# Kernel optimization log

Measured on AMD Instinct MI355X. Metric: run time of the kernel, lower is better.

## Reference

```python
import jax, jax.numpy as jnp
import numpy as np

L, B, D, N = 2048, 8, 1024, 64

def setup_inputs() -> dict:
    key = jax.random.key(0)
    ks = jax.random.split(key, 6)
    return {
        "x": jax.random.normal(ks[0], (L, B, D), dtype=jnp.float32),
        "damping_factor": jax.random.normal(ks[1], (D, N, 1), dtype=jnp.float32),
        "decay_factor": jax.random.normal(ks[2], (D, N, 1), dtype=jnp.float32),
        "ema_expansion_matrix": jax.random.normal(ks[3], (D, N, 1), dtype=jnp.float32),
        "kernel_projection_matrix": jax.random.normal(ks[4], (D, N), dtype=jnp.float32),
        "residual_weight": jax.random.normal(ks[5], (D,), dtype=jnp.float32),
    }

def reference(x, damping_factor, decay_factor, ema_expansion_matrix,
              kernel_projection_matrix, residual_weight):
    seq_len, bsz, dim = x.shape
    ndim = damping_factor.shape[1]
    # --- kernel synthesis (training path, unidirectional) ---
    damping = jax.nn.sigmoid(damping_factor)           # (D, N, 1)
    decay = jax.nn.sigmoid(decay_factor)               # (D, N, 1)
    prev_w = 1.0 - damping * decay                     # (D, N, 1), in (0,1)
    t = jnp.arange(seq_len, dtype=jnp.float32)[None, None, :]  # (1,1,L)
    vander = t * jnp.log(prev_w)                       # (D, N, L)
    kernel_vals = damping * ema_expansion_matrix * jnp.exp(vander)  # (D,N,L)
    kernel = jnp.einsum('dnl,dn->dl', kernel_vals, kernel_projection_matrix)
    kernel = kernel * np.float32(1.0 / np.sqrt(ndim))  # (D, L)
    # --- residual + FFT long convolution ---
    residual = x * residual_weight                     # (L, B, D)
    x_conv = jnp.transpose(x, (1, 2, 0))               # (B, D, L)
    n_fft = 2 * seq_len
    x_fft = jnp.fft.rfft(x_conv, n=n_fft)              # (B, D, n/2+1)
    k_fft = jnp.fft.rfft(kernel, n=n_fft)              # (D, n/2+1)
    conv = jnp.fft.irfft(x_fft * k_fft, n=n_fft)[..., :seq_len]  # (B, D, L)
    ema_out = jnp.transpose(conv, (2, 0, 1))           # (L, B, D)
    return jax.nn.silu(ema_out + residual)
```

## Files before the change

### kernel.cpp

```cpp
#include <hip/hip_runtime.h>
#include <hip/hip_bf16.h>


#define BSZ 8
#define DIM 1024
#define ND 64
#define BD 8192
#define SEGS 4
#define SEGLEN 512
#define CH1 64
#define CPS1 8
#define TD 16
#define XP1 68
#define NCH2 16
#define YP2 17

typedef short bf16x8 __attribute__((ext_vector_type(8)));
typedef float f32x4 __attribute__((ext_vector_type(4)));
union BF8 { uint32_t u[4]; bf16x8 v; };
#define MFMA __builtin_amdgcn_mfma_f32_16x16x32_bf16

__device__ __forceinline__ uint32_t pk_bf16(float a, float b) {
    __hip_bfloat162 h2 = __float22bfloat162_rn(make_float2(a, b));
    uint32_t u; __builtin_memcpy(&u, &h2, 4);
    return u;
}

__device__ __forceinline__ void block_sync_lds() {
    asm volatile("s_waitcnt lgkmcnt(0)" ::: "memory");
    __builtin_amdgcn_s_barrier();
    asm volatile("" ::: "memory");
}

__global__ __launch_bounds__(128, 8) void mega_pass1(
    const float* __restrict__ x,
    const float* __restrict__ dfp,
    const float* __restrict__ cfp,
    ushort* __restrict__ S)
{
    __shared__ float xb[2][TD * XP1];

    const int tid = threadIdx.x;
    const int lane = tid & 63;
    const int wv = tid >> 6;
    const int q   = (lane & 3) | (((lane >> 3) & 1) << 2);
    const int col = wv * 8 + ((lane >> 2) & 1) + ((lane >> 4) & 3) * 2;
    const int blk = blockIdx.x;
    const int dt  = blk & 63;
    const int b   = (blk >> 6) & 7;
    const int seg = blk >> 9;
    const int d   = dt * TD + col;

    float w[8];
    {
        const int pb = d * ND + q * 8;
        const float4 df0 = *(const float4*)(dfp + pb);
        const float4 df1 = *(const float4*)(dfp + pb + 4);
        const float4 cf0 = *(const float4*)(cfp + pb);
        const float4 cf1 = *(const float4*)(cfp + pb + 4);
        const float dfv[8] = {df0.x, df0.y, df0.z, df0.w, df1.x, df1.y, df1.z, df1.w};
        const float cfv[8] = {cf0.x, cf0.y, cf0.z, cf0.w, cf1.x, cf1.y, cf1.z, cf1.w};
        #pragma unroll
        for (int i = 0; i < 8; ++i) {
            const float sd = 1.0f / (1.0f + __expf(-dfv[i]));
            const float sc = 1.0f / (1.0f + __expf(-cfv[i]));
            w[i] = 1.0f - sd * sc;
        }
    }

    const int r0 = tid >> 2;
    const int c4 = (tid & 3) * 4;
    const float* xg = x + (size_t)(seg * SEGLEN) * BD + b * DIM + dt * TD;

    float4 nx0 = *(const float4*)(xg + (size_t)r0 * BD + c4);
    float4 nx1 = *(const float4*)(xg + (size_t)(r0 + 32) * BD + c4);

    float h[8];
    #pragma unroll
    for (int i = 0; i < 8; ++i) h[i] = 0.0f;

    for (int g = 0; g < CPS1; ++g) {
        float* xbuf = xb[g & 1];
        const float nv0[4] = {nx0.x, nx0.y, nx0.z, nx0.w};
        const float nv1[4] = {nx1.x, nx1.y, nx1.z, nx1.w};
        #pragma unroll
        for (int e = 0; e < 4; ++e) {
            xbuf[(c4 + e) * XP1 + r0]      = nv0[e];
            xbuf[(c4 + e) * XP1 + r0 + 32] = nv1[e];
        }
        if (g + 1 < CPS1) {
            nx0 = *(const float4*)(xg + (size_t)((g + 1) * CH1 + r0) * BD + c4);
            nx1 = *(const float4*)(xg + (size_t)((g + 1) * CH1 + r0 + 32) * BD + c4);
        }
        block_sync_lds();

        const float* xcol = xbuf + col * XP1;
        #pragma unroll 2
        for (int t8 = 0; t8 < 8; ++t8) {
            const float4 tva = *(const float4*)(xcol + t8 * 8);
            const float4 tvb = *(const float4*)(xcol + t8 * 8 + 4);
            const float tvs[8] = {tva.x, tva.y, tva.z, tva.w,
                                  tvb.x, tvb.y, tvb.z, tvb.w};
            #pragma unroll
            for (int k = 0; k < 8; ++k) {
                const float xv = tvs[k];
                #pragma unroll
                for (int i = 0; i < 8; ++i) h[i] = fmaf(w[i], h[i], xv);
            }
        }
    }

    const size_t sb = ((size_t)(seg * BSZ + b) * 64 + dt) * 1024 + col * 64 + q * 8;
    uint32_t pk[4] = {pk_bf16(h[0], h[1]), pk_bf16(h[2], h[3]),
                      pk_bf16(h[4], h[5]), pk_bf16(h[6], h[7])};
    *(uint4*)(S + sb) = make_uint4(pk[0], pk[1], pk[2], pk[3]);
}

__global__ __launch_bounds__(1024, 4) void mega_pass2(
    const float* __restrict__ x,
    const float* __restrict__ dfp,
    const float* __restrict__ cfp,
    const float* __restrict__ emp,
    const float* __restrict__ pjp,
    const float* __restrict__ rwp,
    const ushort* __restrict__ S,
    float* __restrict__ out)
{
    __shared__ __align__(16) float   xb[2][TD * 8 * 36];
    __shared__ __align__(16) float   yt[2][256 * YP2];
    __shared__ __align__(16) uint32_t hbq[16 * 256];
    __shared__ __align__(8)  float2  pclw[16 * 64];
    __shared__ float kap[16 * 32];

    const int tid = threadIdx.x;
    const int tl  = tid & 63;
    const int wv  = tid >> 6;
    const int c   = tl & 15;
    const int g   = tl >> 4;
    const int blk = blockIdx.x;
    const int seg = blk >> 6;
    const int dt  = blk & 63;
    const int d0  = dt * TD;
    const int d   = d0 + wv;

    {
        const int pidx = d * ND + tl;
        const float sd = 1.0f / (1.0f + __expf(-dfp[pidx]));
        const float sc = 1.0f / (1.0f + __expf(-cfp[pidx]));
        const float wn = 1.0f - sd * sc;
        const float cn = sd * emp[pidx] * pjp[pidx] * 0.125f;
        pclw[wv * 64 + tl] = make_float2(cn, log2f(wn));
    }
    const float rwd = rwp[d];

    const int rid = tid >> 2;
    const int l_s = rid >> 3;
    const int b_s = rid & 7;
    const int dq  = tid & 3;
    const float* xg_st = x + (size_t)(seg * SEGLEN + l_s) * BD + b_s * DIM + d0 + 4 * dq;
    float4 nx = *(const float4*)(xg_st);

    float lw16[16];
    #pragma unroll
    for (int T = 0; T < 4; ++T)
        #pragma unroll
        for (int r = 0; r < 4; ++r)
            lw16[T * 4 + r] = pclw[wv * 64 + 16 * T + 4 * g + r].y;

    float h[16];
    #pragma unroll
    for (int i = 0; i < 16; ++i) h[i] = 0.0f;
    if (seg > 0) {
        float w512[16];
        #pragma unroll
        for (int i = 0; i < 16; ++i) w512[i] = exp2f(512.0f * lw16[i]);
        for (int sp = 0; sp < seg; ++sp) {
            const size_t sbase = ((size_t)(sp * BSZ + (c & 7)) * 64 + dt) * 1024 + wv * 64;
            #pragma unroll
            for (int T = 0; T < 4; ++T) {
                const uint2 u = *(const uint2*)(S + sbase + 16 * T + 4 * g);
                const float s0 = __uint_as_float(u.x << 16);
                const float s1 = __uint_as_float(u.x & 0xFFFF0000u);
                const float s2 = __uint_as_float(u.y << 16);
                const float s3 = __uint_as_float(u.y & 0xFFFF0000u);
                h[T*4+0] = fmaf(w512[T*4+0], h[T*4+0], s0);
                h[T*4+1] = fmaf(w512[T*4+1], h[T*4+1], s1);
                h[T*4+2] = fmaf(w512[T*4+2], h[T*4+2], s2);
                h[T*4+3] = fmaf(w512[T*4+3], h[T*4+3], s3);
            }
        }
    }
    float w32[16];
    #pragma unroll
    for (int i = 0; i < 16; ++i) w32[i] = exp2f(32.0f * lw16[i]);

    BF8 Vf[4], T2f[2][2], Kf[2];
    #pragma unroll
    for (int T = 0; T < 4; ++T) {
        const float2 pcl = pclw[wv * 64 + 16 * T + c];
        const float winv = exp2f(-pcl.y);
        float ve = exp2f((float)(31 - 8 * g) * pcl.y);
        float vv[8];
        #pragma unroll
        for (int e = 0; e < 8; ++e) { vv[e] = ve; ve *= winv; }
        #pragma unroll
        for (int j = 0; j < 4; ++j) Vf[T].u[j] = pk_bf16(vv[2*j], vv[2*j+1]);
    }
    #pragma unroll
    for (int Tk = 0; Tk < 2; ++Tk) {
        float2 m8[8];
        #pragma unroll
        for (int e = 0; e < 8; ++e) m8[e] = pclw[wv * 64 + 32 * Tk + 8 * g + e];
        #pragma unroll
        for (int Tj = 0; Tj < 2; ++Tj) {
            const float jf = (float)(16 * Tj + c + 1);
            float tv[8];
            #pragma unroll
            for (int e = 0; e < 8; ++e) tv[e] = m8[e].x * exp2f(jf * m8[e].y);
            #pragma unroll
            for (int j = 0; j < 4; ++j) T2f[Tj][Tk].u[j] = pk_bf16(tv[2*j], tv[2*j+1]);
        }
    }
    {
        const int p = tl >> 1, half = tl & 1;
        float acc = 0.0f;
        for (int i = 0; i < 32; ++i) {
            const float2 pc = pclw[wv * 64 + half * 32 + i];
            acc = fmaf(pc.x, exp2f((float)p * pc.y), acc);
        }
        const int prt = __builtin_amdgcn_update_dpp(0, __float_as_int(acc), 0xB1, 0xF, 0xF, true);
        acc += __int_as_float(prt);
        if (!half) kap[wv * 32 + p] = acc;
    }
    #pragma unroll
    for (int Tj = 0; Tj < 2; ++Tj) {
        float kv[8];
        #pragma unroll
        for (int e = 0; e < 8; ++e) {
            const int pp = 16 * Tj + c - 8 * g - e;
            const float kr = kap[wv * 32 + (pp > 0 ? pp : 0)];
            kv[e] = (pp >= 0) ? kr : 0.0f;
        }
        #pragma unroll
        for (int j = 0; j < 4; ++j) Kf[Tj].u[j] = pk_bf16(kv[2*j], kv[2*j+1]);
    }

    const int swl  = (wv >> 2) & 3;
    const int swzc = ((c & 3) << 3) | (((c >> 2) & 1) << 2);
    uint32_t* hbw = hbq + wv * 256 + (c & 7) * 32;
    float* ogbase = out + (size_t)(seg * SEGLEN) * BD + d0;
    const f32x4 zf = {0.0f, 0.0f, 0.0f, 0.0f};

    const int yrho = b_s + 8 * ((l_s >> 2) & 3) + 32 * (l_s & 3) + 128 * (l_s >> 4);

    if (c < 8) {
        #pragma unroll
        for (int T = 0; T < 4; ++T) {
            const uint32_t u0 = pk_bf16(h[4*T+0], h[4*T+1]);
            const uint32_t u1 = pk_bf16(h[4*T+2], h[4*T+3]);
            *(uint2*)(&hbw[(8 * T + 2 * g) ^ swzc]) = make_uint2(u0, u1);
        }
    }
    {
        const float nv[4] = {nx.x, nx.y, nx.z, nx.w};
        #pragma unroll
        for (int e = 0; e < 4; ++e)
            xb[0][((4 * dq + e) * 8 + b_s) * 36 + (l_s ^ (dq << 3))] = nv[e];
        nx = *(const float4*)(xg_st + (size_t)32 * BD);
    }
    block_sync_lds();

    for (int ch = 0; ch < NCH2; ++ch) {
        float* xbuf = xb[ch & 1];
        const float* xrow = xbuf + (wv * 8 + (c & 7)) * 36;

        BF8 hB0, hB1;
        {
            const uint4 a = *(const uint4*)(&hbw[(4 * g) ^ swzc]);
            const uint4 b2 = *(const uint4*)(&hbw[(16 + 4 * g) ^ swzc]);
            hB0.u[0]=a.x; hB0.u[1]=a.y; hB0.u[2]=a.z; hB0.u[3]=a.w;
            hB1.u[0]=b2.x; hB1.u[1]=b2.y; hB1.u[2]=b2.z; hB1.u[3]=b2.w;
        }
        BF8 xB;
        {
            const int kb = (8 * g) ^ (swl << 3);
            const float4 fa = *(const float4*)(xrow + kb);
            const float4 fb = *(const float4*)(xrow + kb + 4);
            xB.u[0] = pk_bf16(fa.x, fa.y); xB.u[1] = pk_bf16(fa.z, fa.w);
            xB.u[2] = pk_bf16(fb.x, fb.y); xB.u[3] = pk_bf16(fb.z, fb.w);
        }

        if (ch + 1 < NCH2) {
            const float nv[4] = {nx.x, nx.y, nx.z, nx.w};
            #pragma unroll
            for (int e = 0; e < 4; ++e)
                xb[(ch + 1) & 1][((4 * dq + e) * 8 + b_s) * 36 + (l_s ^ (dq << 3))] = nv[e];
            if (ch + 2 < NCH2)
                nx = *(const float4*)(xg_st + (size_t)(ch + 2) * 32 * BD);
        }
        if (ch > 0) {
            const float* yprev = yt[(ch - 1) & 1];
            float ov[4];
            #pragma unroll
            for (int e = 0; e < 4; ++e) ov[e] = yprev[yrho * YP2 + 4 * dq + e];
            *(float4*)(ogbase + (size_t)((ch - 1) * 32 + l_s) * BD + b_s * DIM + 4 * dq) =
                make_float4(ov[0], ov[1], ov[2], ov[3]);
        }

        f32x4 y0 = MFMA(Kf[0].v, xB.v, zf, 0, 0, 0);
        f32x4 y1 = MFMA(Kf[1].v, xB.v, zf, 0, 0, 0);
        y0 = MFMA(T2f[0][0].v, hB0.v, y0, 0, 0, 0);
        y1 = MFMA(T2f[1][0].v, hB0.v, y1, 0, 0, 0);
        y0 = MFMA(T2f[0][1].v, hB1.v, y0, 0, 0, 0);
        y1 = MFMA(T2f[1][1].v, hB1.v, y1, 0, 0, 0);
        #pragma unroll
        for (int T = 0; T < 4; ++T) {
            const f32x4 U = MFMA(Vf[T].v, xB.v, zf, 0, 0, 0);
            h[4*T+0] = fmaf(w32[4*T+0], h[4*T+0], U[0]);
            h[4*T+1] = fmaf(w32[4*T+1], h[4*T+1], U[1]);
            h[4*T+2] = fmaf(w32[4*T+2], h[4*T+2], U[2]);
            h[4*T+3] = fmaf(w32[4*T+3], h[4*T+3], U[3]);
        }
        if (c < 8) {
            #pragma unroll
            for (int T = 0; T < 4; ++T) {
                const uint32_t u0 = pk_bf16(h[4*T+0], h[4*T+1]);
                const uint32_t u1 = pk_bf16(h[4*T+2], h[4*T+3]);
                *(uint2*)(&hbw[(8 * T + 2 * g) ^ swzc]) = make_uint2(u0, u1);
            }
        }

        float* ycur = yt[ch & 1];
        #pragma unroll
        for (int Tj = 0; Tj < 2; ++Tj) {
            const int jb = (16 * Tj + 4 * g) ^ (swl << 3);
            const float4 xres = *(const float4*)(xrow + jb);
            const float xr[4] = {xres.x, xres.y, xres.z, xres.w};
            const f32x4 yy = Tj ? y1 : y0;
            #pragma unroll
            for (int r = 0; r < 4; ++r) {
                const float v = yy[r] + rwd * xr[r];
                const float sv = v / (1.0f + __expf(-v));
                if (c < 8)
                    ycur[(c + 8 * (g + 4 * r + 16 * Tj)) * YP2 + wv] = sv;
            }
        }
        block_sync_lds();
    }

    {
        const float* yprev = yt[(NCH2 - 1) & 1];
        float ov[4];
        #pragma unroll
        for (int e = 0; e < 4; ++e) ov[e] = yprev[yrho * YP2 + 4 * dq + e];
        *(float4*)(ogbase + (size_t)((NCH2 - 1) * 32 + l_s) * BD + b_s * DIM + 4 * dq) =
            make_float4(ov[0], ov[1], ov[2], ov[3]);
    }
}

extern "C" void kernel_launch(void* const* d_in, const int* in_sizes, int n_in,
                              void* d_out, int out_size, void* d_ws, size_t ws_size,
                              hipStream_t stream) {
    const float* x  = (const float*)d_in[0];
    const float* df = (const float*)d_in[1];
    const float* cf = (const float*)d_in[2];
    const float* em = (const float*)d_in[3];
    const float* pj = (const float*)d_in[4];
    const float* rw = (const float*)d_in[5];
    float* out = (float*)d_out;
    ushort* S  = (ushort*)d_ws;

    mega_pass1<<<dim3((SEGS - 1) * BSZ * 64), dim3(128), 0, stream>>>(x, df, cf, S);
    mega_pass2<<<dim3(SEGS * 64), dim3(1024), 0, stream>>>(x, df, cf, em, pj, rw, S, out);
}
```

Baseline: 79.04 us.

## Process two 32-step chunks per iteration using idle MFMA column halves

The pass-2 loop now handles 64 timesteps per iteration instead of 32, filling the previously unused upper 8 MFMA columns (c>=8) with a second chunk. The state carry between the two half-chunks is passed via DPP lane moves, and the hidden-state buffer layout and swizzles are reworked. The aim is to halve the loop trip count and barriers and to double useful MFMA work per instruction. In exchange it adds a serial dependency inside each iteration, more LDS usage and extra barrier placement that may lower occupancy.

```diff
diff --git a/kernel.cpp b/kernel.cpp
--- a/kernel.cpp
+++ b/kernel.cpp
@@ -12,8 +12,7 @@
 #define CPS1 8
 #define TD 16
 #define XP1 68
-#define NCH2 16
-#define YP2 17
+#define NIT 8
 
 typedef short bf16x8 __attribute__((ext_vector_type(8)));
 typedef float f32x4 __attribute__((ext_vector_type(4)));
@@ -26,11 +25,18 @@
     return u;
 }
 
+template <int CTRL>
+__device__ __forceinline__ float dpp_mov(float v) {
+    return __int_as_float(__builtin_amdgcn_update_dpp(0, __float_as_int(v), CTRL, 0xF, 0xF, true));
+}
+
 __device__ __forceinline__ void block_sync_lds() {
     asm volatile("s_waitcnt lgkmcnt(0)" ::: "memory");
     __builtin_amdgcn_s_barrier();
     asm volatile("" ::: "memory");
 }
+
+#define HB_ADDR(cc, p0) ((((p0) >> 4) * 256) + ((((p0) >> 2) & 3) * 64) + ((cc) * 4) + ((p0) & 3))
 
 __global__ __launch_bounds__(128, 8) void mega_pass1(
     const float* __restrict__ x,
@@ -126,10 +132,10 @@
     const ushort* __restrict__ S,
     float* __restrict__ out)
 {
-    __shared__ __align__(16) float   xb[2][TD * 8 * 36];
-    __shared__ __align__(16) float   yt[2][256 * YP2];
-    __shared__ __align__(16) uint32_t hbq[16 * 256];
-    __shared__ __align__(8)  float2  pclw[16 * 64];
+    __shared__ __align__(16) float    xb[2][TD * 8 * 68];
+    __shared__ __align__(16) float    yt[512 * 17];
+    __shared__ __align__(16) uint32_t hbq[16 * 512];
+    __shared__ __align__(8)  float2   pclw[16 * 64];
     __shared__ float kap[16 * 32];
 
     const int tid = threadIdx.x;
@@ -137,6 +143,9 @@
     const int wv  = tid >> 6;
     const int c   = tl & 15;
     const int g   = tl >> 4;
+    const int cq  = c & 7;
+    const int hf  = c >> 3;
+    const int swv = (wv >> 2) & 3;
     const int blk = blockIdx.x;
     const int seg = blk >> 6;
     const int dt  = blk & 63;
@@ -158,7 +167,8 @@
     const int b_s = rid & 7;
     const int dq  = tid & 3;
     const float* xg_st = x + (size_t)(seg * SEGLEN + l_s) * BD + b_s * DIM + d0 + 4 * dq;
-    float4 nx = *(const float4*)(xg_st);
+    float4 nxa = *(const float4*)(xg_st);
+    float4 nxb = *(const float4*)(xg_st + (size_t)32 * BD);
 
     float lw16[16];
     #pragma unroll
@@ -175,7 +185,7 @@
         #pragma unroll
         for (int i = 0; i < 16; ++i) w512[i] = exp2f(512.0f * lw16[i]);
         for (int sp = 0; sp < seg; ++sp) {
-            const size_t sbase = ((size_t)(sp * BSZ + (c & 7)) * 64 + dt) * 1024 + wv * 64;
+            const size_t sbase = ((size_t)(sp * BSZ + cq) * 64 + dt) * 1024 + wv * 64;
             #pragma unroll
             for (int T = 0; T < 4; ++T) {
                 const uint2 u = *(const uint2*)(S + sbase + 16 * T + 4 * g);
@@ -245,95 +255,124 @@
         for (int j = 0; j < 4; ++j) Kf[Tj].u[j] = pk_bf16(kv[2*j], kv[2*j+1]);
     }
 
-    const int swl  = (wv >> 2) & 3;
-    const int swzc = ((c & 3) << 3) | (((c >> 2) & 1) << 2);
-    uint32_t* hbw = hbq + wv * 256 + (c & 7) * 32;
+    uint32_t* hbW = hbq + wv * 512;
     float* ogbase = out + (size_t)(seg * SEGLEN) * BD + d0;
     const f32x4 zf = {0.0f, 0.0f, 0.0f, 0.0f};
-
-    const int yrho = b_s + 8 * ((l_s >> 2) & 3) + 32 * (l_s & 3) + 128 * (l_s >> 4);
-
-    if (c < 8) {
+    const int ls_sw = l_s ^ (dq << 3);
+
+    if (hf == 0) {
         #pragma unroll
         for (int T = 0; T < 4; ++T) {
-            const uint32_t u0 = pk_bf16(h[4*T+0], h[4*T+1]);
-            const uint32_t u1 = pk_bf16(h[4*T+2], h[4*T+3]);
-            *(uint2*)(&hbw[(8 * T + 2 * g) ^ swzc]) = make_uint2(u0, u1);
+            const int p0 = 8 * T + 2 * g;
+            *(uint2*)(&hbW[HB_ADDR(c, p0)]) =
+                make_uint2(pk_bf16(h[4*T+0], h[4*T+1]), pk_bf16(h[4*T+2], h[4*T+3]));
         }
     }
     {
-        const float nv[4] = {nx.x, nx.y, nx.z, nx.w};
-        #pragma unroll
-        for (int e = 0; e < 4; ++e)
-            xb[0][((4 * dq + e) * 8 + b_s) * 36 + (l_s ^ (dq << 3))] = nv[e];
-        nx = *(const float4*)(xg_st + (size_t)32 * BD);
+        const float va[4] = {nxa.x, nxa.y, nxa.z, nxa.w};
+        const float vb[4] = {nxb.x, nxb.y, nxb.z, nxb.w};
+        #pragma unroll
+        for (int e = 0; e < 4; ++e) {
+            xb[0][(4*dq + e) * 544 + b_s * 68 + ls_sw]      = va[e];
+            xb[0][(4*dq + e) * 544 + b_s * 68 + ls_sw + 32] = vb[e];
+        }
+        nxa = *(const float4*)(xg_st + (size_t)64 * BD);
+        nxb = *(const float4*)(xg_st + (size_t)96 * BD);
     }
     block_sync_lds();
 
-    for (int ch = 0; ch < NCH2; ++ch) {
-        float* xbuf = xb[ch & 1];
-        const float* xrow = xbuf + (wv * 8 + (c & 7)) * 36;
-
-        BF8 hB0, hB1;
-        {
-            const uint4 a = *(const uint4*)(&hbw[(4 * g) ^ swzc]);
-            const uint4 b2 = *(const uint4*)(&hbw[(16 + 4 * g) ^ swzc]);
-            hB0.u[0]=a.x; hB0.u[1]=a.y; hB0.u[2]=a.z; hB0.u[3]=a.w;
-            hB1.u[0]=b2.x; hB1.u[1]=b2.y; hB1.u[2]=b2.z; hB1.u[3]=b2.w;
-        }
+    for (int it = 0; it < NIT; ++it) {
+        if (it > 0) {
+            #pragma unroll
+            for (int hh = 0; hh < 2; ++hh) {
+                const int l6 = l_s + 32 * hh;
+                const int sig = ((l6 >> 2) & 3) + 4 * (l6 & 3) + 16 * ((l6 >> 4) & 1) + 32 * (l6 >> 5);
+                const int rho = b_s + 8 * sig;
+                float ov[4];
+                #pragma unroll
+                for (int e = 0; e < 4; ++e) ov[e] = yt[rho * 17 + 4 * dq + e];
+                *(float4*)(ogbase + (size_t)((it - 1) * 64 + l6) * BD + b_s * DIM + 4 * dq) =
+                    make_float4(ov[0], ov[1], ov[2], ov[3]);
+            }
+        }
+        if (it + 1 < NIT) {
+            float* xbn = xb[(it + 1) & 1];
+            const float va[4] = {nxa.x, nxa.y, nxa.z, nxa.w};
+            const float vb[4] = {nxb.x, nxb.y, nxb.z, nxb.w};
+            #pragma unroll
+            for (int e = 0; e < 4; ++e) {
+                xbn[(4*dq + e) * 544 + b_s * 68 + ls_sw]      = va[e];
+                xbn[(4*dq + e) * 544 + b_s * 68 + ls_sw + 32] = vb[e];
+            }
+            if (it + 2 < NIT) {
+                nxa = *(const float4*)(xg_st + (size_t)(it + 2) * 64 * BD);
+                nxb = *(const float4*)(xg_st + (size_t)((it + 2) * 64 + 32) * BD);
+            }
+        }
+        block_sync_lds();
+
+        const float* xrow = xb[it & 1] + wv * 544 + cq * 68 + hf * 32;
         BF8 xB;
         {
-            const int kb = (8 * g) ^ (swl << 3);
+            const int kb = 8 * (g ^ swv);
             const float4 fa = *(const float4*)(xrow + kb);
             const float4 fb = *(const float4*)(xrow + kb + 4);
             xB.u[0] = pk_bf16(fa.x, fa.y); xB.u[1] = pk_bf16(fa.z, fa.w);
             xB.u[2] = pk_bf16(fb.x, fb.y); xB.u[3] = pk_bf16(fb.z, fb.w);
         }
 
-        if (ch + 1 < NCH2) {
-            const float nv[4] = {nx.x, nx.y, nx.z, nx.w};
-            #pragma unroll
-            for (int e = 0; e < 4; ++e)
-                xb[(ch + 1) & 1][((4 * dq + e) * 8 + b_s) * 36 + (l_s ^ (dq << 3))] = nv[e];
-            if (ch + 2 < NCH2)
-                nx = *(const float4*)(xg_st + (size_t)(ch + 2) * 32 * BD);
-        }
-        if (ch > 0) {
-            const float* yprev = yt[(ch - 1) & 1];
-            float ov[4];
-            #pragma unroll
-            for (int e = 0; e < 4; ++e) ov[e] = yprev[yrho * YP2 + 4 * dq + e];
-            *(float4*)(ogbase + (size_t)((ch - 1) * 32 + l_s) * BD + b_s * DIM + 4 * dq) =
-                make_float4(ov[0], ov[1], ov[2], ov[3]);
-        }
-
+        f32x4 Uf[4];
+        #pragma unroll
+        for (int T = 0; T < 4; ++T) Uf[T] = MFMA(Vf[T].v, xB.v, zf, 0, 0, 0);
         f32x4 y0 = MFMA(Kf[0].v, xB.v, zf, 0, 0, 0);
         f32x4 y1 = MFMA(Kf[1].v, xB.v, zf, 0, 0, 0);
+
+        float hb_[16], uB_[16];
+        #pragma unroll
+        for (int T = 0; T < 4; ++T) {
+            #pragma unroll
+            for (int r = 0; r < 4; ++r) {
+                const float u = Uf[T][r];
+                const float t = dpp_mov<0x128>(u);
+                const float uA = hf ? t : u;
+                uB_[4*T+r] = hf ? u : t;
+                hb_[4*T+r] = fmaf(w32[4*T+r], h[4*T+r], uA);
+            }
+        }
+        if (hf) {
+            #pragma unroll
+            for (int T = 0; T < 4; ++T) {
+                const int p0 = 8 * T + 2 * g;
+                *(uint2*)(&hbW[HB_ADDR(c, p0)]) =
+                    make_uint2(pk_bf16(hb_[4*T+0], hb_[4*T+1]), pk_bf16(hb_[4*T+2], hb_[4*T+3]));
+            }
+        }
+        BF8 hB0, hB1;
+        {
+            const uint4 a  = *(const uint4*)(&hbW[g * 64 + c * 4]);
+            const uint4 b2 = *(const uint4*)(&hbW[256 + g * 64 + c * 4]);
+            hB0.u[0]=a.x;  hB0.u[1]=a.y;  hB0.u[2]=a.z;  hB0.u[3]=a.w;
+            hB1.u[0]=b2.x; hB1.u[1]=b2.y; hB1.u[2]=b2.z; hB1.u[3]=b2.w;
+        }
         y0 = MFMA(T2f[0][0].v, hB0.v, y0, 0, 0, 0);
         y1 = MFMA(T2f[1][0].v, hB0.v, y1, 0, 0, 0);
         y0 = MFMA(T2f[0][1].v, hB1.v, y0, 0, 0, 0);
         y1 = MFMA(T2f[1][1].v, hB1.v, y1, 0, 0, 0);
-        #pragma unroll
-        for (int T = 0; T < 4; ++T) {
-            const f32x4 U = MFMA(Vf[T].v, xB.v, zf, 0, 0, 0);
-            h[4*T+0] = fmaf(w32[4*T+0], h[4*T+0], U[0]);
-            h[4*T+1] = fmaf(w32[4*T+1], h[4*T+1], U[1]);
-            h[4*T+2] = fmaf(w32[4*T+2], h[4*T+2], U[2]);
-            h[4*T+3] = fmaf(w32[4*T+3], h[4*T+3], U[3]);
-        }
-        if (c < 8) {
+
+        #pragma unroll
+        for (int i = 0; i < 16; ++i) h[i] = fmaf(w32[i], hb_[i], uB_[i]);
+        if (!hf) {
             #pragma unroll
             for (int T = 0; T < 4; ++T) {
-                const uint32_t u0 = pk_bf16(h[4*T+0], h[4*T+1]);
-                const uint32_t u1 = pk_bf16(h[4*T+2], h[4*T+3]);
-                *(uint2*)(&hbw[(8 * T + 2 * g) ^ swzc]) = make_uint2(u0, u1);
-            }
-        }
-
-        float* ycur = yt[ch & 1];
+                const int p0 = 8 * T + 2 * g;
+                *(uint2*)(&hbW[HB_ADDR(c, p0)]) =
+                    make_uint2(pk_bf16(h[4*T+0], h[4*T+1]), pk_bf16(h[4*T+2], h[4*T+3]));
+            }
+        }
+
         #pragma unroll
         for (int Tj = 0; Tj < 2; ++Tj) {
-            const int jb = (16 * Tj + 4 * g) ^ (swl << 3);
+            const int jb = 16 * (Tj ^ (swv >> 1)) + 4 * (g ^ ((swv & 1) << 1));
             const float4 xres = *(const float4*)(xrow + jb);
             const float xr[4] = {xres.x, xres.y, xres.z, xres.w};
             const f32x4 yy = Tj ? y1 : y0;
@@ -341,20 +380,25 @@
             for (int r = 0; r < 4; ++r) {
                 const float v = yy[r] + rwd * xr[r];
                 const float sv = v / (1.0f + __expf(-v));
-                if (c < 8)
-                    ycur[(c + 8 * (g + 4 * r + 16 * Tj)) * YP2 + wv] = sv;
+                const int rho = cq + 8 * (g + 4 * r + 16 * Tj + 32 * hf);
+                yt[rho * 17 + wv] = sv;
             }
         }
         block_sync_lds();
     }
 
     {
-        const float* yprev = yt[(NCH2 - 1) & 1];
-        float ov[4];
-        #pragma unroll
-        for (int e = 0; e < 4; ++e) ov[e] = yprev[yrho * YP2 + 4 * dq + e];
-        *(float4*)(ogbase + (size_t)((NCH2 - 1) * 32 + l_s) * BD + b_s * DIM + 4 * dq) =
-            make_float4(ov[0], ov[1], ov[2], ov[3]);
+        #pragma unroll
+        for (int hh = 0; hh < 2; ++hh) {
+            const int l6 = l_s + 32 * hh;
+            const int sig = ((l6 >> 2) & 3) + 4 * (l6 & 3) + 16 * ((l6 >> 4) & 1) + 32 * (l6 >> 5);
+            const int rho = b_s + 8 * sig;
+            float ov[4];
+            #pragma unroll
+            for (int e = 0; e < 4; ++e) ov[e] = yt[rho * 17 + 4 * dq + e];
+            *(float4*)(ogbase + (size_t)((NIT - 1) * 64 + l6) * BD + b_s * DIM + 4 * dq) =
+                make_float4(ov[0], ov[1], ov[2], ov[3]);
+        }
     }
 }
 
```

After: 116.6 us. 47.5% more time.
